# Optimization experiments

Hardware: AMD Instinct MI355X
Metric: run time of the kernel (lower is better)

## Reference

```python
import jax, jax.numpy as jnp
import numpy as np

N_NODES = 100000
N_EDGES = 1600000
D_IN = 64
D_OUT = 64


def setup_inputs() -> dict:
    key = jax.random.key(0)
    k1, k2, k3, k4, k5, k6, k7 = jax.random.split(key, 7)
    x = jax.random.normal(k1, (N_NODES, D_IN), dtype=jnp.float32)
    edge_index = jax.random.randint(k2, (2, N_EDGES), 0, N_NODES, dtype=jnp.int64)
    pos_encoding = jax.random.normal(k3, (N_NODES, D_IN), dtype=jnp.float32)
    # GCNConv linear weight (no bias inside lin; bias added post-aggregation)
    W_gcn = jax.random.normal(k4, (D_IN, D_OUT), dtype=jnp.float32) / np.sqrt(D_IN)
    b_gcn = jax.random.normal(k5, (D_OUT,), dtype=jnp.float32) * 0.01
    # positional encoding Linear
    W_pos = jax.random.normal(k6, (D_IN, D_OUT), dtype=jnp.float32) / np.sqrt(D_IN)
    b_pos = jax.random.normal(k7, (D_OUT,), dtype=jnp.float32) * 0.01
    return {"x": x, "edge_index": edge_index, "pos_encoding": pos_encoding,
            "W_gcn": W_gcn, "b_gcn": b_gcn, "W_pos": W_pos, "b_pos": b_pos}


def _gcn_conv(x, edge_index, W, b):
    n = x.shape[0]
    # add self-loops (PyG GCNConv default)
    loop = jnp.arange(n, dtype=edge_index.dtype)
    src = jnp.concatenate([edge_index[0], loop])
    dst = jnp.concatenate([edge_index[1], loop])
    # symmetric normalization: deg over destination with unit edge weights
    deg = jax.ops.segment_sum(jnp.ones_like(src, dtype=x.dtype), dst, num_segments=n)
    dinv = jnp.where(deg > 0, jax.lax.rsqrt(deg), 0.0)
    norm = dinv[src] * dinv[dst]  # [E+N]
    h = x @ W  # [N, D_OUT]
    msg = h[src] * norm[:, None]  # gather + scale
    out = jax.ops.segment_sum(msg, dst, num_segments=n)  # scatter-add
    return out + b


def reference(x, edge_index, pos_encoding, W_gcn, b_gcn, W_pos, b_pos):
    conv_out = _gcn_conv(x, edge_index, W_gcn, b_gcn)
    pos = pos_encoding @ W_pos + b_pos
    return conv_out + pos
```

## Files before the change

kernel.cpp:

```cpp
#include <hip/hip_runtime.h>
#include <hip/hip_fp16.h>

#define NN 100000
#define NE 1600000
#define D  64

#define SB    256
#define CHUNK 6250
#define BSH   7
#define BMSK  127
#define NB    782
#define PAD   784
#define CAPS  2560

typedef __attribute__((ext_vector_type(8))) _Float16 f16x8;
typedef __attribute__((ext_vector_type(4))) float    f32x4;

__device__ __forceinline__ void scan_bsum_wave0(const int* __restrict__ bsum,
                                                int* binoff_l, int t) {
    if (t < 64) {
        int base = t * 13;
        int loc[13]; int run = 0;
#pragma unroll
        for (int j = 0; j < 13; ++j) {
            int idx = base + j;
            int v = (idx < NB) ? bsum[idx] : 0;
            loc[j] = run; run += v;
        }
        int pre = run;
#pragma unroll
        for (int off = 1; off < 64; off <<= 1) {
            int u = __shfl_up(pre, off);
            if (t >= off) pre += u;
        }
        pre -= run;
#pragma unroll
        for (int j = 0; j < 13; ++j) {
            int idx = base + j;
            if (idx <= NB) binoff_l[idx] = pre + loc[j];
        }
    }
}

__global__ __launch_bounds__(1024) void k_hist(const int* __restrict__ dst,
                                               int* __restrict__ hist) {
    __shared__ int h[NB];
    int t = threadIdx.x, blk = blockIdx.x;
    for (int i = t; i < NB; i += 1024) h[i] = 0;
    __syncthreads();
    int e0 = blk * CHUNK;
    for (int e = e0 + t; e < e0 + CHUNK; e += 1024)
        atomicAdd(&h[dst[e] >> BSH], 1);
    __syncthreads();
    for (int i = t; i < NB; i += 1024) hist[blk * PAD + i] = h[i];
}

__global__ __launch_bounds__(256) void k_scanT(int* __restrict__ hist,
                                               int* __restrict__ bsum) {
    __shared__ int ps[8][256];
    int t = threadIdx.x, b0 = blockIdx.x * 8;
    int v[8];
#pragma unroll
    for (int j = 0; j < 8; ++j) {
        v[j] = (b0 + j < NB) ? hist[t * PAD + b0 + j] : 0;
        ps[j][t] = v[j];
    }
    __syncthreads();
    for (int off = 1; off < 256; off <<= 1) {
        int u[8];
#pragma unroll
        for (int j = 0; j < 8; ++j) u[j] = (t >= off) ? ps[j][t - off] : 0;
        __syncthreads();
#pragma unroll
        for (int j = 0; j < 8; ++j) ps[j][t] += u[j];
        __syncthreads();
    }
#pragma unroll
    for (int j = 0; j < 8; ++j)
        if (b0 + j < NB) hist[t * PAD + b0 + j] = ps[j][t] - v[j];
    if (t == 255) {
#pragma unroll
        for (int j = 0; j < 8; ++j)
            if (b0 + j < NB) bsum[b0 + j] = ps[j][t];
    }
}

__global__ __launch_bounds__(1024) void k_scatter1(
    const int* __restrict__ src, const int* __restrict__ dst,
    const int* __restrict__ hist, const int* __restrict__ bsum,
    unsigned* __restrict__ ebuf)
{
    __shared__ int cur[NB];
    __shared__ int binoff_l[NB + 1];
    int t = threadIdx.x, blk = blockIdx.x;
    scan_bsum_wave0(bsum, binoff_l, t);
    __syncthreads();
    for (int i = t; i < NB; i += 1024)
        cur[i] = binoff_l[i] + hist[blk * PAD + i];
    __syncthreads();
    int e0 = blk * CHUNK;
    for (int e = e0 + t; e < e0 + CHUNK; e += 1024) {
        int d = dst[e];
        int p = atomicAdd(&cur[d >> BSH], 1);
        ebuf[p] = ((unsigned)src[e] << BSH) | (unsigned)(d & BMSK);
    }
}

__global__ __launch_bounds__(512) void k_count(const int* __restrict__ bsum,
                                               const unsigned* __restrict__ ebuf,
                                               float* __restrict__ dinv) {
    __shared__ int c[128];
    __shared__ int binoff_l[NB + 1];
    int t = threadIdx.x, b = blockIdx.x;
    scan_bsum_wave0(bsum, binoff_l, t);
    if (t < 128) c[t] = 0;
    __syncthreads();
    int e0 = binoff_l[b], e1 = binoff_l[b + 1];
    for (int e = e0 + t; e < e1; e += 512)
        atomicAdd(&c[ebuf[e] & BMSK], 1);
    __syncthreads();
    if (t < 128) {
        int node = (b << BSH) + t;
        if (node < NN) dinv[node] = rsqrtf((float)(c[t] + 1));
    }
}

__global__ __launch_bounds__(256) void k_mm(
    const float* __restrict__ x, const float* __restrict__ Wg,
    const float* __restrict__ dinv, __half* __restrict__ g,
    const float* __restrict__ pos, const float* __restrict__ Wp,
    const float* __restrict__ bg, const float* __restrict__ bp,
    float* __restrict__ out)
{
    __shared__ __align__(16) _Float16 Wt[64][64];
    int t = threadIdx.x;
    int lane = t & 63;
    int wid = t >> 6;
    int half_grid = gridDim.x >> 1;
    bool job2 = blockIdx.x >= half_grid;
    int blk = job2 ? (blockIdx.x - half_grid) : blockIdx.x;
    const float* A = job2 ? pos : x;
    const float* W = job2 ? Wp : Wg;

    if (blockIdx.x == 0 && t < 64) g[(long)NN * D + t] = __float2half(0.f);

    for (int i = t; i < 64 * 64; i += 256) {
        int k = i >> 6, n = i & 63;
        Wt[n][k] = (_Float16)W[i];
    }
    __syncthreads();

    int lr = lane & 15;
    int lg = lane >> 4;
    int kofs = lg * 8;

    f16x8 b[4][2];
#pragma unroll
    for (int n = 0; n < 4; ++n)
#pragma unroll
        for (int kt = 0; kt < 2; ++kt)
            b[n][kt] = *(const f16x8*)&Wt[n * 16 + lr][kt * 32 + kofs];

    float bsv[4] = {0.f, 0.f, 0.f, 0.f};
    if (job2) {
#pragma unroll
        for (int n = 0; n < 4; ++n) {
            int cc = n * 16 + lr;
            bsv[n] = bg[cc] + bp[cc];
        }
    }

    for (int rb0 = blk * 64; rb0 < NN; rb0 += half_grid * 64) {
        int rb = rb0 + wid * 16;
        int arow = rb + lr;
        int arc = arow < NN ? arow : NN - 1;
        const float4* ap = (const float4*)(A + (long)arc * 64 + kofs);
        float4 p0 = ap[0], p1 = ap[1], p2 = ap[8], p3 = ap[9];
        f16x8 a0, a1;
        a0[0] = (_Float16)p0.x; a0[1] = (_Float16)p0.y;
        a0[2] = (_Float16)p0.z; a0[3] = (_Float16)p0.w;
        a0[4] = (_Float16)p1.x; a0[5] = (_Float16)p1.y;
        a0[6] = (_Float16)p1.z; a0[7] = (_Float16)p1.w;
        a1[0] = (_Float16)p2.x; a1[1] = (_Float16)p2.y;
        a1[2] = (_Float16)p2.z; a1[3] = (_Float16)p2.w;
        a1[4] = (_Float16)p3.x; a1[5] = (_Float16)p3.y;
        a1[6] = (_Float16)p3.z; a1[7] = (_Float16)p3.w;

        f32x4 z = {0.f, 0.f, 0.f, 0.f};
        f32x4 acc[4] = {z, z, z, z};
#pragma unroll
        for (int n = 0; n < 4; ++n) {
            acc[n] = __builtin_amdgcn_mfma_f32_16x16x32_f16(a0, b[n][0], acc[n], 0, 0, 0);
            acc[n] = __builtin_amdgcn_mfma_f32_16x16x32_f16(a1, b[n][1], acc[n], 0, 0, 0);
        }

        int orow0 = rb + lg * 4;
        if (!job2) {
#pragma unroll
            for (int r = 0; r < 4; ++r) {
                int row = orow0 + r;
                if (row < NN) {
                    float di = dinv[row];
#pragma unroll
                    for (int n = 0; n < 4; ++n)
                        g[(long)row * D + n * 16 + lr] = __float2half(acc[n][r] * di);
                }
            }
        } else {
#pragma unroll
            for (int r = 0; r < 4; ++r) {
                int row = orow0 + r;
                if (row < NN) {
#pragma unroll
                    for (int n = 0; n < 4; ++n)
                        out[(long)row * D + n * 16 + lr] = acc[n][r] + bsv[n];
                }
            }
        }
    }
}

__global__ __launch_bounds__(512) void k_gather(
    const int* __restrict__ bsum, unsigned* __restrict__ ebuf,
    const __half* __restrict__ g, float* __restrict__ out)
{
    __shared__ unsigned cache[CAPS];
    __shared__ int c[128];
    __shared__ int cur[128];
    __shared__ int rs_l[129];
    __shared__ int binoff_l[NB + 1];
    int t = threadIdx.x, b = blockIdx.x;
    int lane = t & 63, w = t >> 6;

    scan_bsum_wave0(bsum, binoff_l, t);
    if (t < 128) c[t] = 0;
    __syncthreads();
    int e0 = binoff_l[b];
    int cnt = binoff_l[b + 1] - e0;

    for (int i = t; i < cnt; i += 512) {
        unsigned u = ebuf[e0 + i];
        if (i < CAPS) cache[i] = u;
        atomicAdd(&c[u & BMSK], 1);
    }
    __syncthreads();

    if (t < 64) {
        int l0 = c[2 * t], l1 = c[2 * t + 1];
        int run = l0 + l1;
        int pre = run;
#pragma unroll
        for (int off = 1; off < 64; off <<= 1) {
            int u = __shfl_up(pre, off);
            if (t >= off) pre += u;
        }
        pre -= run;
        rs_l[2 * t] = pre;        cur[2 * t] = pre;
        rs_l[2 * t + 1] = pre + l0; cur[2 * t + 1] = pre + l0;
        if (t == 63) rs_l[128] = pre + run;
    }

    unsigned ur[8]; int nmy = 0;
    for (int i = t, j = 0; i < cnt && j < 8; i += 512, ++j) {
        ur[j] = (i < CAPS) ? cache[i] : ebuf[e0 + i];
        nmy = j + 1;
    }
    __syncthreads();
    for (int j = 0; j < nmy; ++j) {
        unsigned u = ur[j];
        int p = atomicAdd(&cur[u & BMSK], 1);
        unsigned s = u >> BSH;
        if (p < CAPS) cache[p] = s; else ebuf[e0 + p] = s;
    }
    __syncthreads();

    int f = lane & 7;
    int grp = lane >> 3;
    const uint4* gq = (const uint4*)g;
    for (int p = 0; p < 16; ++p) {
        int r = p * 8 + w;
        int node = (b << BSH) + r;
        if (node >= NN) continue;
        int rs0 = rs_l[r];
        int nl = rs_l[r + 1] - rs0;
        float a0 = 0.f, a1 = 0.f, a2 = 0.f, a3 = 0.f;
        float a4 = 0.f, a5 = 0.f, a6 = 0.f, a7 = 0.f;
        int NG = (nl + 7) >> 3;
        for (int c2 = 0; c2 < NG; ++c2) {
            int idx = c2 * 8 + grp;
            int s = NN;
            if (idx < nl) {
                int ii = rs0 + idx;
                s = (ii < CAPS) ? (int)cache[ii] : (int)ebuf[e0 + ii];
            }
            uint4 u = gq[(long)s * 8 + f];
            __half2 h0 = *(__half2*)&u.x, h1 = *(__half2*)&u.y;
            __half2 h2 = *(__half2*)&u.z, h3 = *(__half2*)&u.w;
            a0 += __low2float(h0); a1 += __high2float(h0);
            a2 += __low2float(h1); a3 += __high2float(h1);
            a4 += __low2float(h2); a5 += __high2float(h2);
            a6 += __low2float(h3); a7 += __high2float(h3);
        }
#pragma unroll
        for (int mask = 8; mask <= 32; mask <<= 1) {
            a0 += __shfl_xor(a0, mask); a1 += __shfl_xor(a1, mask);
            a2 += __shfl_xor(a2, mask); a3 += __shfl_xor(a3, mask);
            a4 += __shfl_xor(a4, mask); a5 += __shfl_xor(a5, mask);
            a6 += __shfl_xor(a6, mask); a7 += __shfl_xor(a7, mask);
        }
        if (lane < 16) {
            int ff = lane & 7, hs = lane >> 3;
            uint4 u = gq[(long)node * 8 + ff];
            __half2 s0 = hs ? *(__half2*)&u.z : *(__half2*)&u.x;
            __half2 s1 = hs ? *(__half2*)&u.w : *(__half2*)&u.y;
            float b0 = hs ? a4 : a0, b1 = hs ? a5 : a1;
            float b2 = hs ? a6 : a2, b3 = hs ? a7 : a3;
            float di = rsqrtf((float)(c[r] + 1));
            float4* op = (float4*)(out + (long)node * D) + (ff * 2 + hs);
            float4 o = *op;
            o.x += (b0 + __low2float(s0)) * di;
            o.y += (b1 + __high2float(s0)) * di;
            o.z += (b2 + __low2float(s1)) * di;
            o.w += (b3 + __high2float(s1)) * di;
            *op = o;
        }
    }
}

extern "C" void kernel_launch(void* const* d_in, const int* in_sizes, int n_in,
                              void* d_out, int out_size, void* d_ws, size_t ws_size,
                              hipStream_t stream) {
    const float* x   = (const float*)d_in[0];
    const int*   ei  = (const int*)d_in[1];
    const float* pos = (const float*)d_in[2];
    const float* Wg  = (const float*)d_in[3];
    const float* bg  = (const float*)d_in[4];
    const float* Wp  = (const float*)d_in[5];
    const float* bp  = (const float*)d_in[6];
    float* out = (float*)d_out;

    const int* src = ei;
    const int* dst = ei + NE;

    char* Wb = (char*)d_ws;
    unsigned* ebuf = (unsigned*)Wb;
    __half*   g    = (__half*)(Wb + 6400000);
    int*      hist = (int*)(Wb + 19200128);
    int*      bsum = hist + SB * PAD;
    float*    dinv = (float*)(bsum + 784);

    hipLaunchKernelGGL(k_hist,     dim3(SB),   dim3(1024), 0, stream, dst, hist);
    hipLaunchKernelGGL(k_scanT,    dim3(98),   dim3(256),  0, stream, hist, bsum);
    hipLaunchKernelGGL(k_scatter1, dim3(SB),   dim3(1024), 0, stream,
                       src, dst, hist, bsum, ebuf);
    hipLaunchKernelGGL(k_count,    dim3(NB),   dim3(512),  0, stream,
                       bsum, ebuf, dinv);
    hipLaunchKernelGGL(k_mm,       dim3(1564), dim3(256),  0, stream,
                       x, Wg, dinv, g, pos, Wp, bg, bp, out);
    hipLaunchKernelGGL(k_gather,   dim3(NB),   dim3(512),  0, stream,
                       bsum, ebuf, g, out);
}
```

Measured before the change: 207.6 us.

## Fuse positional linear into gather kernel and rewrite bin scan with wave shuffles

Moves the pos_encoding @ W_pos projection out of the matmul kernel and into the gather kernel. Each 128-node bin now stages its aggregated GCN rows in shared memory, runs the positional projection with MFMA, and writes the output once. This removes the read-modify-write of the output buffer and the separate write pass for the positional term. The transposed histogram scan is also rewritten to use 32 bins per 1024-thread block with wave-shuffle prefix sums instead of a barrier-heavy Hillis-Steele loop, and the matmul grid is resized. In exchange, the gather kernel uses much more shared memory (about 35KB for gres plus 8KB for weights), which may reduce its occupancy.

Result: slower. 220.6 us (+6.3%).

```diff
diff --git a/kernel.cpp b/kernel.cpp
--- a/kernel.cpp
+++ b/kernel.cpp
@@ -12,6 +12,7 @@
 #define NB    782
 #define PAD   784
 #define CAPS  2560
+#define GPD   68
 
 typedef __attribute__((ext_vector_type(8))) _Float16 f16x8;
 typedef __attribute__((ext_vector_type(4))) float    f32x4;
@@ -55,33 +56,40 @@
     for (int i = t; i < NB; i += 1024) hist[blk * PAD + i] = h[i];
 }
 
-__global__ __launch_bounds__(256) void k_scanT(int* __restrict__ hist,
-                                               int* __restrict__ bsum) {
-    __shared__ int ps[8][256];
-    int t = threadIdx.x, b0 = blockIdx.x * 8;
-    int v[8];
-#pragma unroll
-    for (int j = 0; j < 8; ++j) {
-        v[j] = (b0 + j < NB) ? hist[t * PAD + b0 + j] : 0;
-        ps[j][t] = v[j];
-    }
-    __syncthreads();
-    for (int off = 1; off < 256; off <<= 1) {
-        int u[8];
-#pragma unroll
-        for (int j = 0; j < 8; ++j) u[j] = (t >= off) ? ps[j][t - off] : 0;
-        __syncthreads();
-#pragma unroll
-        for (int j = 0; j < 8; ++j) ps[j][t] += u[j];
-        __syncthreads();
-    }
-#pragma unroll
-    for (int j = 0; j < 8; ++j)
-        if (b0 + j < NB) hist[t * PAD + b0 + j] = ps[j][t] - v[j];
-    if (t == 255) {
-#pragma unroll
-        for (int j = 0; j < 8; ++j)
-            if (b0 + j < NB) bsum[b0 + j] = ps[j][t];
+__global__ __launch_bounds__(1024) void k_scanT(int* __restrict__ hist,
+                                                int* __restrict__ bsum) {
+    __shared__ int ps[256][33];
+    int t = threadIdx.x, b0 = blockIdx.x * 32;
+    for (int i = t; i < 256 * 32; i += 1024) {
+        int r = i >> 5, cc = i & 31;
+        int bin = b0 + cc;
+        ps[r][cc] = (bin < NB) ? hist[r * PAD + bin] : 0;
+    }
+    __syncthreads();
+    int w = t >> 6, lane = t & 63;
+    for (int cc = w; cc < 32; cc += 16) {
+        int base = lane * 4;
+        int v0 = ps[base][cc], v1 = ps[base + 1][cc];
+        int v2 = ps[base + 2][cc], v3 = ps[base + 3][cc];
+        int run = v0 + v1 + v2 + v3;
+        int pre = run;
+#pragma unroll
+        for (int off = 1; off < 64; off <<= 1) {
+            int u = __shfl_up(pre, off);
+            if (lane >= off) pre += u;
+        }
+        pre -= run;
+        ps[base][cc]     = pre;
+        ps[base + 1][cc] = pre + v0;
+        ps[base + 2][cc] = pre + v0 + v1;
+        ps[base + 3][cc] = pre + v0 + v1 + v2;
+        if (lane == 63 && b0 + cc < NB) bsum[b0 + cc] = pre + run;
+    }
+    __syncthreads();
+    for (int i = t; i < 256 * 32; i += 1024) {
+        int r = i >> 5, cc = i & 31;
+        int bin = b0 + cc;
+        if (bin < NB) hist[r * PAD + bin] = ps[r][cc];
     }
 }
 
@@ -127,31 +135,22 @@
 
 __global__ __launch_bounds__(256) void k_mm(
     const float* __restrict__ x, const float* __restrict__ Wg,
-    const float* __restrict__ dinv, __half* __restrict__ g,
-    const float* __restrict__ pos, const float* __restrict__ Wp,
-    const float* __restrict__ bg, const float* __restrict__ bp,
-    float* __restrict__ out)
+    const float* __restrict__ dinv, __half* __restrict__ g)
 {
     __shared__ __align__(16) _Float16 Wt[64][64];
     int t = threadIdx.x;
     int lane = t & 63;
     int wid = t >> 6;
-    int half_grid = gridDim.x >> 1;
-    bool job2 = blockIdx.x >= half_grid;
-    int blk = job2 ? (blockIdx.x - half_grid) : blockIdx.x;
-    const float* A = job2 ? pos : x;
-    const float* W = job2 ? Wp : Wg;
 
     if (blockIdx.x == 0 && t < 64) g[(long)NN * D + t] = __float2half(0.f);
 
     for (int i = t; i < 64 * 64; i += 256) {
         int k = i >> 6, n = i & 63;
-        Wt[n][k] = (_Float16)W[i];
-    }
-    __syncthreads();
-
-    int lr = lane & 15;
-    int lg = lane >> 4;
+        Wt[n][k] = (_Float16)Wg[i];
+    }
+    __syncthreads();
+
+    int lr = lane & 15, lg = lane >> 4;
     int kofs = lg * 8;
 
     f16x8 b[4][2];
@@ -161,20 +160,11 @@
         for (int kt = 0; kt < 2; ++kt)
             b[n][kt] = *(const f16x8*)&Wt[n * 16 + lr][kt * 32 + kofs];
 
-    float bsv[4] = {0.f, 0.f, 0.f, 0.f};
-    if (job2) {
-#pragma unroll
-        for (int n = 0; n < 4; ++n) {
-            int cc = n * 16 + lr;
-            bsv[n] = bg[cc] + bp[cc];
-        }
-    }
-
-    for (int rb0 = blk * 64; rb0 < NN; rb0 += half_grid * 64) {
+    for (int rb0 = blockIdx.x * 64; rb0 < NN; rb0 += gridDim.x * 64) {
         int rb = rb0 + wid * 16;
         int arow = rb + lr;
         int arc = arow < NN ? arow : NN - 1;
-        const float4* ap = (const float4*)(A + (long)arc * 64 + kofs);
+        const float4* ap = (const float4*)(x + (long)arc * 64 + kofs);
         float4 p0 = ap[0], p1 = ap[1], p2 = ap[8], p3 = ap[9];
         f16x8 a0, a1;
         a0[0] = (_Float16)p0.x; a0[1] = (_Float16)p0.y;
@@ -195,26 +185,14 @@
         }
 
         int orow0 = rb + lg * 4;
-        if (!job2) {
-#pragma unroll
-            for (int r = 0; r < 4; ++r) {
-                int row = orow0 + r;
-                if (row < NN) {
-                    float di = dinv[row];
-#pragma unroll
-                    for (int n = 0; n < 4; ++n)
-                        g[(long)row * D + n * 16 + lr] = __float2half(acc[n][r] * di);
-                }
-            }
-        } else {
-#pragma unroll
-            for (int r = 0; r < 4; ++r) {
-                int row = orow0 + r;
-                if (row < NN) {
-#pragma unroll
-                    for (int n = 0; n < 4; ++n)
-                        out[(long)row * D + n * 16 + lr] = acc[n][r] + bsv[n];
-                }
+#pragma unroll
+        for (int r = 0; r < 4; ++r) {
+            int row = orow0 + r;
+            if (row < NN) {
+                float di = dinv[row];
+#pragma unroll
+                for (int n = 0; n < 4; ++n)
+                    g[(long)row * D + n * 16 + lr] = __float2half(acc[n][r] * di);
             }
         }
     }
@@ -222,9 +200,14 @@
 
 __global__ __launch_bounds__(512) void k_gather(
     const int* __restrict__ bsum, unsigned* __restrict__ ebuf,
-    const __half* __restrict__ g, float* __restrict__ out)
+    const __half* __restrict__ g,
+    const float* __restrict__ pos, const float* __restrict__ Wp,
+    const float* __restrict__ bg, const float* __restrict__ bp,
+    float* __restrict__ out)
 {
     __shared__ unsigned cache[CAPS];
+    __shared__ float gres[128 * GPD];
+    __shared__ __align__(16) _Float16 Wt[64][64];
     __shared__ int c[128];
     __shared__ int cur[128];
     __shared__ int rs_l[129];
@@ -232,6 +215,10 @@
     int t = threadIdx.x, b = blockIdx.x;
     int lane = t & 63, w = t >> 6;
 
+    for (int i = t; i < 64 * 64; i += 512) {
+        int k = i >> 6, n = i & 63;
+        Wt[n][k] = (_Float16)Wp[i];
+    }
     scan_bsum_wave0(bsum, binoff_l, t);
     if (t < 128) c[t] = 0;
     __syncthreads();
@@ -255,7 +242,7 @@
             if (t >= off) pre += u;
         }
         pre -= run;
-        rs_l[2 * t] = pre;        cur[2 * t] = pre;
+        rs_l[2 * t] = pre;          cur[2 * t] = pre;
         rs_l[2 * t + 1] = pre + l0; cur[2 * t + 1] = pre + l0;
         if (t == 63) rs_l[128] = pre + run;
     }
@@ -316,13 +303,62 @@
             float b0 = hs ? a4 : a0, b1 = hs ? a5 : a1;
             float b2 = hs ? a6 : a2, b3 = hs ? a7 : a3;
             float di = rsqrtf((float)(c[r] + 1));
-            float4* op = (float4*)(out + (long)node * D) + (ff * 2 + hs);
-            float4 o = *op;
-            o.x += (b0 + __low2float(s0)) * di;
-            o.y += (b1 + __high2float(s0)) * di;
-            o.z += (b2 + __low2float(s1)) * di;
-            o.w += (b3 + __high2float(s1)) * di;
-            *op = o;
+            float4 o;
+            o.x = (b0 + __low2float(s0)) * di;
+            o.y = (b1 + __high2float(s0)) * di;
+            o.z = (b2 + __low2float(s1)) * di;
+            o.w = (b3 + __high2float(s1)) * di;
+            *(float4*)&gres[r * GPD + (ff * 2 + hs) * 4] = o;
+        }
+    }
+    __syncthreads();
+
+    int lr = lane & 15, lg = lane >> 4;
+    int kofs = lg * 8;
+    f16x8 bfr[4][2];
+#pragma unroll
+    for (int n = 0; n < 4; ++n)
+#pragma unroll
+        for (int kt = 0; kt < 2; ++kt)
+            bfr[n][kt] = *(const f16x8*)&Wt[n * 16 + lr][kt * 32 + kofs];
+    float bias[4];
+#pragma unroll
+    for (int n = 0; n < 4; ++n) {
+        int cc = n * 16 + lr;
+        bias[n] = bg[cc] + bp[cc];
+    }
+    int node0 = (b << BSH);
+    int rb = w * 16;
+    int arow = node0 + rb + lr;
+    int arc = arow < NN ? arow : NN - 1;
+    const float4* ap = (const float4*)(pos + (long)arc * 64 + kofs);
+    float4 p0 = ap[0], p1 = ap[1], p2 = ap[8], p3 = ap[9];
+    f16x8 a0, a1;
+    a0[0] = (_Float16)p0.x; a0[1] = (_Float16)p0.y;
+    a0[2] = (_Float16)p0.z; a0[3] = (_Float16)p0.w;
+    a0[4] = (_Float16)p1.x; a0[5] = (_Float16)p1.y;
+    a0[6] = (_Float16)p1.z; a0[7] = (_Float16)p1.w;
+    a1[0] = (_Float16)p2.x; a1[1] = (_Float16)p2.y;
+    a1[2] = (_Float16)p2.z; a1[3] = (_Float16)p2.w;
+    a1[4] = (_Float16)p3.x; a1[5] = (_Float16)p3.y;
+    a1[6] = (_Float16)p3.z; a1[7] = (_Float16)p3.w;
+    f32x4 z = {0.f, 0.f, 0.f, 0.f};
+    f32x4 acc[4] = {z, z, z, z};
+#pragma unroll
+    for (int n = 0; n < 4; ++n) {
+        acc[n] = __builtin_amdgcn_mfma_f32_16x16x32_f16(a0, bfr[n][0], acc[n], 0, 0, 0);
+        acc[n] = __builtin_amdgcn_mfma_f32_16x16x32_f16(a1, bfr[n][1], acc[n], 0, 0, 0);
+    }
+    int orow0 = rb + lg * 4;
+#pragma unroll
+    for (int r = 0; r < 4; ++r) {
+        int row = orow0 + r;
+        int node = node0 + row;
+        if (node < NN) {
+#pragma unroll
+            for (int n = 0; n < 4; ++n)
+                out[(long)node * 64 + n * 16 + lr] =
+                    acc[n][r] + bias[n] + gres[row * GPD + n * 16 + lr];
         }
     }
 }
@@ -350,13 +386,13 @@
     float*    dinv = (float*)(bsum + 784);
 
     hipLaunchKernelGGL(k_hist,     dim3(SB),   dim3(1024), 0, stream, dst, hist);
-    hipLaunchKernelGGL(k_scanT,    dim3(98),   dim3(256),  0, stream, hist, bsum);
+    hipLaunchKernelGGL(k_scanT,    dim3(25),   dim3(1024), 0, stream, hist, bsum);
     hipLaunchKernelGGL(k_scatter1, dim3(SB),   dim3(1024), 0, stream,
                        src, dst, hist, bsum, ebuf);
     hipLaunchKernelGGL(k_count,    dim3(NB),   dim3(512),  0, stream,
                        bsum, ebuf, dinv);
-    hipLaunchKernelGGL(k_mm,       dim3(1564), dim3(256),  0, stream,
-                       x, Wg, dinv, g, pos, Wp, bg, bp, out);
+    hipLaunchKernelGGL(k_mm,       dim3(1024), dim3(256),  0, stream,
+                       x, Wg, dinv, g);
     hipLaunchKernelGGL(k_gather,   dim3(NB),   dim3(512),  0, stream,
-                       bsum, ebuf, g, out);
-}
+                       bsum, ebuf, g, pos, Wp, bg, bp, out);
+}
```

## Fuse histogram, scan, scatter and degree count into one cooperative kernel

Applied to the files above, without the earlier changes.

Replaces four separate preprocessing launches (hist, transposed scan, scatter, count) with a single cooperative kernel that uses grid.sync between phases. It shares one union of shared memory across phases, and the scan is redone with 32 bins per block using wave shuffles. The aim is to remove launch overhead and inter-kernel gaps. The cost is grid-wide barriers, fewer blocks doing the scan and count phases, and a dependence on all 256 blocks being co-resident.

After: 560.3 us. +169.9%, slower.

```diff
diff --git a/kernel.cpp b/kernel.cpp
--- a/kernel.cpp
+++ b/kernel.cpp
@@ -1,5 +1,8 @@
 #include <hip/hip_runtime.h>
 #include <hip/hip_fp16.h>
+#include <hip/hip_cooperative_groups.h>
+
+namespace cg = cooperative_groups;
 
 #define NN 100000
 #define NE 1600000
@@ -42,86 +45,95 @@
     }
 }
 
-__global__ __launch_bounds__(1024) void k_hist(const int* __restrict__ dst,
-                                               int* __restrict__ hist) {
-    __shared__ int h[NB];
+union PrepSM {
+    int h[NB];
+    int ps[256][33];
+    int cur[NB];
+    int c[128];
+};
+
+__global__ __launch_bounds__(1024) void k_prep(
+    const int* __restrict__ src, const int* __restrict__ dst,
+    int* __restrict__ hist, int* __restrict__ bsum,
+    unsigned* __restrict__ ebuf, float* __restrict__ dinv)
+{
+    __shared__ PrepSM sm;
+    __shared__ int binoff_l[NB + 1];
+    cg::grid_group grid = cg::this_grid();
     int t = threadIdx.x, blk = blockIdx.x;
-    for (int i = t; i < NB; i += 1024) h[i] = 0;
-    __syncthreads();
     int e0 = blk * CHUNK;
+
+    for (int i = t; i < NB; i += 1024) sm.h[i] = 0;
+    __syncthreads();
     for (int e = e0 + t; e < e0 + CHUNK; e += 1024)
-        atomicAdd(&h[dst[e] >> BSH], 1);
-    __syncthreads();
-    for (int i = t; i < NB; i += 1024) hist[blk * PAD + i] = h[i];
-}
-
-__global__ __launch_bounds__(256) void k_scanT(int* __restrict__ hist,
-                                               int* __restrict__ bsum) {
-    __shared__ int ps[8][256];
-    int t = threadIdx.x, b0 = blockIdx.x * 8;
-    int v[8];
-#pragma unroll
-    for (int j = 0; j < 8; ++j) {
-        v[j] = (b0 + j < NB) ? hist[t * PAD + b0 + j] : 0;
-        ps[j][t] = v[j];
-    }
-    __syncthreads();
-    for (int off = 1; off < 256; off <<= 1) {
-        int u[8];
-#pragma unroll
-        for (int j = 0; j < 8; ++j) u[j] = (t >= off) ? ps[j][t - off] : 0;
-        __syncthreads();
-#pragma unroll
-        for (int j = 0; j < 8; ++j) ps[j][t] += u[j];
-        __syncthreads();
-    }
-#pragma unroll
-    for (int j = 0; j < 8; ++j)
-        if (b0 + j < NB) hist[t * PAD + b0 + j] = ps[j][t] - v[j];
-    if (t == 255) {
-#pragma unroll
-        for (int j = 0; j < 8; ++j)
-            if (b0 + j < NB) bsum[b0 + j] = ps[j][t];
-    }
-}
-
-__global__ __launch_bounds__(1024) void k_scatter1(
-    const int* __restrict__ src, const int* __restrict__ dst,
-    const int* __restrict__ hist, const int* __restrict__ bsum,
-    unsigned* __restrict__ ebuf)
-{
-    __shared__ int cur[NB];
-    __shared__ int binoff_l[NB + 1];
-    int t = threadIdx.x, blk = blockIdx.x;
+        atomicAdd(&sm.h[dst[e] >> BSH], 1);
+    __syncthreads();
+    for (int i = t; i < NB; i += 1024) hist[blk * PAD + i] = sm.h[i];
+    __threadfence();
+    grid.sync();
+
+    if (blk < 25) {
+        int b0 = blk * 32;
+        for (int i = t; i < 256 * 32; i += 1024) {
+            int r = i >> 5, cc = i & 31;
+            int bin = b0 + cc;
+            sm.ps[r][cc] = (bin < NB) ? hist[r * PAD + bin] : 0;
+        }
+        __syncthreads();
+        int w = t >> 6, lane = t & 63;
+        for (int cc = w; cc < 32; cc += 16) {
+            int base = lane * 4;
+            int v0 = sm.ps[base][cc], v1 = sm.ps[base + 1][cc];
+            int v2 = sm.ps[base + 2][cc], v3 = sm.ps[base + 3][cc];
+            int run = v0 + v1 + v2 + v3;
+            int pre = run;
+#pragma unroll
+            for (int off = 1; off < 64; off <<= 1) {
+                int u = __shfl_up(pre, off);
+                if (lane >= off) pre += u;
+            }
+            pre -= run;
+            sm.ps[base][cc]     = pre;
+            sm.ps[base + 1][cc] = pre + v0;
+            sm.ps[base + 2][cc] = pre + v0 + v1;
+            sm.ps[base + 3][cc] = pre + v0 + v1 + v2;
+            if (lane == 63 && b0 + cc < NB) bsum[b0 + cc] = pre + run;
+        }
+        __syncthreads();
+        for (int i = t; i < 256 * 32; i += 1024) {
+            int r = i >> 5, cc = i & 31;
+            int bin = b0 + cc;
+            if (bin < NB) hist[r * PAD + bin] = sm.ps[r][cc];
+        }
+    }
+    __threadfence();
+    grid.sync();
+
     scan_bsum_wave0(bsum, binoff_l, t);
     __syncthreads();
     for (int i = t; i < NB; i += 1024)
-        cur[i] = binoff_l[i] + hist[blk * PAD + i];
-    __syncthreads();
-    int e0 = blk * CHUNK;
+        sm.cur[i] = binoff_l[i] + hist[blk * PAD + i];
+    __syncthreads();
     for (int e = e0 + t; e < e0 + CHUNK; e += 1024) {
         int d = dst[e];
-        int p = atomicAdd(&cur[d >> BSH], 1);
+        int p = atomicAdd(&sm.cur[d >> BSH], 1);
         ebuf[p] = ((unsigned)src[e] << BSH) | (unsigned)(d & BMSK);
     }
-}
-
-__global__ __launch_bounds__(512) void k_count(const int* __restrict__ bsum,
-                                               const unsigned* __restrict__ ebuf,
-                                               float* __restrict__ dinv) {
-    __shared__ int c[128];
-    __shared__ int binoff_l[NB + 1];
-    int t = threadIdx.x, b = blockIdx.x;
-    scan_bsum_wave0(bsum, binoff_l, t);
-    if (t < 128) c[t] = 0;
-    __syncthreads();
-    int e0 = binoff_l[b], e1 = binoff_l[b + 1];
-    for (int e = e0 + t; e < e1; e += 512)
-        atomicAdd(&c[ebuf[e] & BMSK], 1);
-    __syncthreads();
-    if (t < 128) {
-        int node = (b << BSH) + t;
-        if (node < NN) dinv[node] = rsqrtf((float)(c[t] + 1));
+    __threadfence();
+    grid.sync();
+
+    for (int b = blk; b < NB; b += SB) {
+        if (t < 128) sm.c[t] = 0;
+        __syncthreads();
+        int s0 = binoff_l[b], s1 = binoff_l[b + 1];
+        for (int e = s0 + t; e < s1; e += 1024)
+            atomicAdd(&sm.c[ebuf[e] & BMSK], 1);
+        __syncthreads();
+        if (t < 128) {
+            int node = (b << BSH) + t;
+            if (node < NN) dinv[node] = rsqrtf((float)(sm.c[t] + 1));
+        }
+        __syncthreads();
     }
 }
 
@@ -255,7 +267,7 @@
             if (t >= off) pre += u;
         }
         pre -= run;
-        rs_l[2 * t] = pre;        cur[2 * t] = pre;
+        rs_l[2 * t] = pre;          cur[2 * t] = pre;
         rs_l[2 * t + 1] = pre + l0; cur[2 * t + 1] = pre + l0;
         if (t == 63) rs_l[128] = pre + run;
     }
@@ -349,14 +361,12 @@
     int*      bsum = hist + SB * PAD;
     float*    dinv = (float*)(bsum + 784);
 
-    hipLaunchKernelGGL(k_hist,     dim3(SB),   dim3(1024), 0, stream, dst, hist);
-    hipLaunchKernelGGL(k_scanT,    dim3(98),   dim3(256),  0, stream, hist, bsum);
-    hipLaunchKernelGGL(k_scatter1, dim3(SB),   dim3(1024), 0, stream,
-                       src, dst, hist, bsum, ebuf);
-    hipLaunchKernelGGL(k_count,    dim3(NB),   dim3(512),  0, stream,
-                       bsum, ebuf, dinv);
-    hipLaunchKernelGGL(k_mm,       dim3(1564), dim3(256),  0, stream,
+    void* prep_args[] = {(void*)&src, (void*)&dst, (void*)&hist,
+                         (void*)&bsum, (void*)&ebuf, (void*)&dinv};
+    hipLaunchCooperativeKernel((void*)k_prep, dim3(SB), dim3(1024),
+                               prep_args, 0, stream);
+    hipLaunchKernelGGL(k_mm,     dim3(1564), dim3(256), 0, stream,
                        x, Wg, dinv, g, pos, Wp, bg, bp, out);
-    hipLaunchKernelGGL(k_gather,   dim3(NB),   dim3(512),  0, stream,
+    hipLaunchKernelGGL(k_gather, dim3(NB),   dim3(512), 0, stream,
                        bsum, ebuf, g, out);
 }
```

## Assign one node per 8-lane group in gather and rewrite scan with wave shuffles

Applied to the files above, without the earlier changes.

The gather kernel now gives each group of 8 lanes its own destination node and walks that node's edge list serially, instead of spreading a node's edges across a whole wave and reducing with cross-lane shuffles. This removes the shuffle reductions and the idle lanes left on nodes with few edges, at the cost of load imbalance between groups whose nodes have different degrees. The column scan kernel is reworked to scan 32 bins per 1024-thread block using wave shuffle prefix sums over a padded shared tile. This replaces the Hillis-Steele loop with its many block barriers and uses fewer, larger blocks.

Measured after the change: 187.8 us. -9.5%, faster.

```diff
diff --git a/kernel.cpp b/kernel.cpp
--- a/kernel.cpp
+++ b/kernel.cpp
@@ -55,33 +55,40 @@
     for (int i = t; i < NB; i += 1024) hist[blk * PAD + i] = h[i];
 }
 
-__global__ __launch_bounds__(256) void k_scanT(int* __restrict__ hist,
-                                               int* __restrict__ bsum) {
-    __shared__ int ps[8][256];
-    int t = threadIdx.x, b0 = blockIdx.x * 8;
-    int v[8];
-#pragma unroll
-    for (int j = 0; j < 8; ++j) {
-        v[j] = (b0 + j < NB) ? hist[t * PAD + b0 + j] : 0;
-        ps[j][t] = v[j];
-    }
-    __syncthreads();
-    for (int off = 1; off < 256; off <<= 1) {
-        int u[8];
-#pragma unroll
-        for (int j = 0; j < 8; ++j) u[j] = (t >= off) ? ps[j][t - off] : 0;
-        __syncthreads();
-#pragma unroll
-        for (int j = 0; j < 8; ++j) ps[j][t] += u[j];
-        __syncthreads();
-    }
-#pragma unroll
-    for (int j = 0; j < 8; ++j)
-        if (b0 + j < NB) hist[t * PAD + b0 + j] = ps[j][t] - v[j];
-    if (t == 255) {
-#pragma unroll
-        for (int j = 0; j < 8; ++j)
-            if (b0 + j < NB) bsum[b0 + j] = ps[j][t];
+__global__ __launch_bounds__(1024) void k_scanT(int* __restrict__ hist,
+                                                int* __restrict__ bsum) {
+    __shared__ int ps[256][33];
+    int t = threadIdx.x, b0 = blockIdx.x * 32;
+    for (int i = t; i < 256 * 32; i += 1024) {
+        int r = i >> 5, cc = i & 31;
+        int bin = b0 + cc;
+        ps[r][cc] = (bin < NB) ? hist[r * PAD + bin] : 0;
+    }
+    __syncthreads();
+    int w = t >> 6, lane = t & 63;
+    for (int cc = w; cc < 32; cc += 16) {
+        int base = lane * 4;
+        int v0 = ps[base][cc], v1 = ps[base + 1][cc];
+        int v2 = ps[base + 2][cc], v3 = ps[base + 3][cc];
+        int run = v0 + v1 + v2 + v3;
+        int pre = run;
+#pragma unroll
+        for (int off = 1; off < 64; off <<= 1) {
+            int u = __shfl_up(pre, off);
+            if (lane >= off) pre += u;
+        }
+        pre -= run;
+        ps[base][cc]     = pre;
+        ps[base + 1][cc] = pre + v0;
+        ps[base + 2][cc] = pre + v0 + v1;
+        ps[base + 3][cc] = pre + v0 + v1 + v2;
+        if (lane == 63 && b0 + cc < NB) bsum[b0 + cc] = pre + run;
+    }
+    __syncthreads();
+    for (int i = t; i < 256 * 32; i += 1024) {
+        int r = i >> 5, cc = i & 31;
+        int bin = b0 + cc;
+        if (bin < NB) hist[r * PAD + bin] = ps[r][cc];
     }
 }
 
@@ -255,7 +262,7 @@
             if (t >= off) pre += u;
         }
         pre -= run;
-        rs_l[2 * t] = pre;        cur[2 * t] = pre;
+        rs_l[2 * t] = pre;          cur[2 * t] = pre;
         rs_l[2 * t + 1] = pre + l0; cur[2 * t + 1] = pre + l0;
         if (t == 63) rs_l[128] = pre + run;
     }
@@ -277,52 +284,42 @@
     int f = lane & 7;
     int grp = lane >> 3;
     const uint4* gq = (const uint4*)g;
-    for (int p = 0; p < 16; ++p) {
-        int r = p * 8 + w;
+#pragma unroll
+    for (int half = 0; half < 2; ++half) {
+        int r = w * 16 + half * 8 + grp;
         int node = (b << BSH) + r;
-        if (node >= NN) continue;
-        int rs0 = rs_l[r];
-        int nl = rs_l[r + 1] - rs0;
-        float a0 = 0.f, a1 = 0.f, a2 = 0.f, a3 = 0.f;
-        float a4 = 0.f, a5 = 0.f, a6 = 0.f, a7 = 0.f;
-        int NG = (nl + 7) >> 3;
-        for (int c2 = 0; c2 < NG; ++c2) {
-            int idx = c2 * 8 + grp;
-            int s = NN;
-            if (idx < nl) {
-                int ii = rs0 + idx;
-                s = (ii < CAPS) ? (int)cache[ii] : (int)ebuf[e0 + ii];
+        if (node < NN) {
+            int rs0 = rs_l[r];
+            int nl = rs_l[r + 1] - rs0;
+            float a0 = 0.f, a1 = 0.f, a2 = 0.f, a3 = 0.f;
+            float a4 = 0.f, a5 = 0.f, a6 = 0.f, a7 = 0.f;
+#pragma unroll 4
+            for (int k = 0; k < nl; ++k) {
+                int ii = rs0 + k;
+                int s = (ii < CAPS) ? (int)cache[ii] : (int)ebuf[e0 + ii];
+                uint4 u = gq[s * 8 + f];
+                __half2 h0 = *(__half2*)&u.x, h1 = *(__half2*)&u.y;
+                __half2 h2 = *(__half2*)&u.z, h3 = *(__half2*)&u.w;
+                a0 += __low2float(h0); a1 += __high2float(h0);
+                a2 += __low2float(h1); a3 += __high2float(h1);
+                a4 += __low2float(h2); a5 += __high2float(h2);
+                a6 += __low2float(h3); a7 += __high2float(h3);
             }
-            uint4 u = gq[(long)s * 8 + f];
-            __half2 h0 = *(__half2*)&u.x, h1 = *(__half2*)&u.y;
-            __half2 h2 = *(__half2*)&u.z, h3 = *(__half2*)&u.w;
-            a0 += __low2float(h0); a1 += __high2float(h0);
-            a2 += __low2float(h1); a3 += __high2float(h1);
-            a4 += __low2float(h2); a5 += __high2float(h2);
-            a6 += __low2float(h3); a7 += __high2float(h3);
-        }
-#pragma unroll
-        for (int mask = 8; mask <= 32; mask <<= 1) {
-            a0 += __shfl_xor(a0, mask); a1 += __shfl_xor(a1, mask);
-            a2 += __shfl_xor(a2, mask); a3 += __shfl_xor(a3, mask);
-            a4 += __shfl_xor(a4, mask); a5 += __shfl_xor(a5, mask);
-            a6 += __shfl_xor(a6, mask); a7 += __shfl_xor(a7, mask);
-        }
-        if (lane < 16) {
-            int ff = lane & 7, hs = lane >> 3;
-            uint4 u = gq[(long)node * 8 + ff];
-            __half2 s0 = hs ? *(__half2*)&u.z : *(__half2*)&u.x;
-            __half2 s1 = hs ? *(__half2*)&u.w : *(__half2*)&u.y;
-            float b0 = hs ? a4 : a0, b1 = hs ? a5 : a1;
-            float b2 = hs ? a6 : a2, b3 = hs ? a7 : a3;
             float di = rsqrtf((float)(c[r] + 1));
-            float4* op = (float4*)(out + (long)node * D) + (ff * 2 + hs);
-            float4 o = *op;
-            o.x += (b0 + __low2float(s0)) * di;
-            o.y += (b1 + __high2float(s0)) * di;
-            o.z += (b2 + __low2float(s1)) * di;
-            o.w += (b3 + __high2float(s1)) * di;
-            *op = o;
+            uint4 su = gq[node * 8 + f];
+            __half2 s0 = *(__half2*)&su.x, s1 = *(__half2*)&su.y;
+            __half2 s2 = *(__half2*)&su.z, s3 = *(__half2*)&su.w;
+            float4* op = (float4*)(out + node * 64 + f * 8);
+            float4 o0 = op[0], o1 = op[1];
+            o0.x += (a0 + __low2float(s0)) * di;
+            o0.y += (a1 + __high2float(s0)) * di;
+            o0.z += (a2 + __low2float(s1)) * di;
+            o0.w += (a3 + __high2float(s1)) * di;
+            o1.x += (a4 + __low2float(s2)) * di;
+            o1.y += (a5 + __high2float(s2)) * di;
+            o1.z += (a6 + __low2float(s3)) * di;
+            o1.w += (a7 + __high2float(s3)) * di;
+            op[0] = o0; op[1] = o1;
         }
     }
 }
@@ -350,7 +347,7 @@
     float*    dinv = (float*)(bsum + 784);
 
     hipLaunchKernelGGL(k_hist,     dim3(SB),   dim3(1024), 0, stream, dst, hist);
-    hipLaunchKernelGGL(k_scanT,    dim3(98),   dim3(256),  0, stream, hist, bsum);
+    hipLaunchKernelGGL(k_scanT,    dim3(25),   dim3(1024), 0, stream, hist, bsum);
     hipLaunchKernelGGL(k_scatter1, dim3(SB),   dim3(1024), 0, stream,
                        src, dst, hist, bsum, ebuf);
     hipLaunchKernelGGL(k_count,    dim3(NB),   dim3(512),  0, stream,
```
